# Performance work log

Hardware: AMD Instinct MI355X
Metric: run time of the kernel (lower is better)

## Reference

```python
import jax, jax.numpy as jnp
import numpy as np

B, S, EMB = 2, 2048, 4096
NHEADS, KVHEADS, HEAD_D = 32, 8, 128
SPLITS = (NHEADS * HEAD_D, KVHEADS * HEAD_D, KVHEADS * HEAD_D)  # 4096, 1024, 1024


def setup_inputs() -> dict:
    key = jax.random.key(0)
    k1, k2, k3 = jax.random.split(key, 3)
    q = jax.random.normal(k1, (B, S, EMB), dtype=jnp.float32)
    # nn.Linear weights, torch layout [out_features, in_features], std=0.02 init
    w_qkv = jax.random.normal(k2, (sum(SPLITS), EMB), dtype=jnp.float32) * 0.02
    w_dense = jax.random.normal(k3, (EMB, NHEADS * HEAD_D), dtype=jnp.float32) * 0.02
    return {"q": q, "w_qkv": w_qkv, "w_dense": w_dense}


def reference(q, w_qkv, w_dense):
    # Self-attention path of PagedMultiHeadAttention (no cache), causal mask.
    Bq, Sq, _ = q.shape
    qkv = q @ w_qkv.T                                  # [B, S, 6144]
    qs, ks, vs = jnp.split(qkv, np.cumsum(SPLITS)[:-1], axis=-1)
    G = NHEADS // KVHEADS                              # GQA expansion = 4
    # queries grouped per kv-head: [B, S, KVH, G, D]
    qh = qs.reshape(Bq, Sq, KVHEADS, G, HEAD_D)
    kh = ks.reshape(Bq, Sq, KVHEADS, HEAD_D)
    vh = vs.reshape(Bq, Sq, KVHEADS, HEAD_D)
    scale = 1.0 / jnp.sqrt(jnp.float32(HEAD_D))
    scores = jnp.einsum("bskgd,btkd->bkgst", qh, kh) * scale  # [B,KVH,G,S,S]
    causal = jnp.tril(jnp.ones((Sq, Sq), dtype=bool))
    scores = jnp.where(causal, scores, jnp.finfo(scores.dtype).min)
    probs = jax.nn.softmax(scores, axis=-1)
    attn = jnp.einsum("bkgst,btkd->bskgd", probs, vh)  # [B,S,KVH,G,D]
    attn = attn.reshape(Bq, Sq, NHEADS * HEAD_D)
    return attn @ w_dense.T                            # [B, S, EMB]
```

## Files before the change

kernel.cpp:

```cpp
#include <hip/hip_runtime.h>
#include <hip/hip_bf16.h>

typedef __bf16 bf16x8 __attribute__((ext_vector_type(8)));
typedef __bf16 bf16x4 __attribute__((ext_vector_type(4)));
typedef float  f32x4  __attribute__((ext_vector_type(4)));

typedef __attribute__((address_space(3))) void lds_vp;
typedef const __attribute__((address_space(1))) void gbl_vp;

__global__ void cast_f32_bf16(const float* __restrict__ src, __bf16* __restrict__ dst, int n8) {
    int i = blockIdx.x * 256 + threadIdx.x;
    if (i >= n8) return;
    const float4* s = (const float4*)src;
    float4 a = s[2 * i], b = s[2 * i + 1];
    bf16x8 o;
    o[0] = (__bf16)a.x; o[1] = (__bf16)a.y; o[2] = (__bf16)a.z; o[3] = (__bf16)a.w;
    o[4] = (__bf16)b.x; o[5] = (__bf16)b.y; o[6] = (__bf16)b.z; o[7] = (__bf16)b.w;
    ((bf16x8*)dst)[i] = o;
}


__device__ __forceinline__ void stage_half(const __bf16* __restrict__ g, int K, int kt,
                                           __bf16* lds_tile, int h, int w, int l) {
#pragma unroll
    for (int j = 0; j < 2; ++j) {
        const int rih = (j * 8 + w) * 8 + (l >> 3);
        const __bf16* src = g + (size_t)(h * 128 + rih) * K + kt * 64 + (((l & 7) ^ (l >> 3)) << 3);
        __bf16* dst = lds_tile + h * 8192 + (j * 8 + w) * 512;
        __builtin_amdgcn_global_load_lds((gbl_vp*)src, (lds_vp*)dst, 16, 0, 0);
    }
}

__device__ __forceinline__ bf16x8 lds_frag(const __bf16* base, int row, int kb) {
    return *(const bf16x8*)((const char*)base + row * 128 + (kb ^ ((row & 7) << 4)));
}

template <int OUT_BF16>
__global__ __launch_bounds__(512, 2)
void gemm256(const __bf16* __restrict__ A, const __bf16* __restrict__ Bm,
             void* __restrict__ Cout, int M, int N, int K) {
    __shared__ __bf16 As[2][256 * 64];
    __shared__ __bf16 Bs[2][256 * 64];
    const int tid = threadIdx.x;
    const int lane = tid & 63, wid = tid >> 6;
    const int g = lane >> 4, lq = lane & 15;
    const int wm = wid >> 2, wn = wid & 3;
    const size_t brow = (size_t)blockIdx.y * 256, bcol = (size_t)blockIdx.x * 256;
    const __bf16* Ag = A + brow * K;
    const __bf16* Bg = Bm + bcol * K;
    const int nkt = K >> 6, niter = nkt >> 1;

    f32x4 acc[8][4] = {};

    stage_half(Ag, K, 0, &As[0][0], 0, wid, lane);
    stage_half(Bg, K, 0, &Bs[0][0], 0, wid, lane);
    stage_half(Ag, K, 0, &As[0][0], 1, wid, lane);
    stage_half(Bg, K, 0, &Bs[0][0], 1, wid, lane);

    const int arow0 = wm * 128 + lq;
    const int brow0 = wn * 64 + lq;

    for (int it = 0; it < niter; ++it) {
        const int t0 = 2 * it;
#pragma unroll
        for (int hf = 0; hf < 2; ++hf) {
            const __bf16* SA = &As[hf][0];
            const __bf16* SB = &Bs[hf][0];
            __bf16* DA = &As[hf ^ 1][0];
            __bf16* DB = &Bs[hf ^ 1][0];
            const int tstage = t0 + 1 + hf;
            const bool dostage = (tstage < nkt);
            bf16x8 bfr[4][2];

            if (dostage) stage_half(Ag, K, tstage, DA, 0, wid, lane);
            __builtin_amdgcn_sched_barrier(0);
            if (dostage) asm volatile("s_waitcnt vmcnt(2)" ::: "memory");
            else         asm volatile("s_waitcnt vmcnt(0)" ::: "memory");
            __builtin_amdgcn_s_barrier();
            __builtin_amdgcn_sched_barrier(0);
#pragma unroll
            for (int n = 0; n < 4; ++n)
#pragma unroll
                for (int kk = 0; kk < 2; ++kk)
                    bfr[n][kk] = lds_frag(SB, brow0 + n * 16, kk * 64 + g * 16);
            {
                bf16x8 afr[2][2];
#pragma unroll
                for (int mm = 0; mm < 2; ++mm)
#pragma unroll
                    for (int kk = 0; kk < 2; ++kk)
                        afr[mm][kk] = lds_frag(SA, arow0 + mm * 16, kk * 64 + g * 16);
                __builtin_amdgcn_s_setprio(1);
#pragma unroll
                for (int kk = 0; kk < 2; ++kk)
#pragma unroll
                    for (int n = 0; n < 4; ++n)
#pragma unroll
                        for (int mm = 0; mm < 2; ++mm)
                            acc[mm][n] = __builtin_amdgcn_mfma_f32_16x16x32_bf16(afr[mm][kk], bfr[n][kk], acc[mm][n], 0, 0, 0);
                __builtin_amdgcn_s_setprio(0);
            }
            __builtin_amdgcn_sched_barrier(0);
            __builtin_amdgcn_s_barrier();
            __builtin_amdgcn_sched_barrier(0);

#pragma unroll
            for (int q = 1; q < 4; ++q) {
                bf16x8 afr[2][2];
#pragma unroll
                for (int mm = 0; mm < 2; ++mm)
#pragma unroll
                    for (int kk = 0; kk < 2; ++kk)
                        afr[mm][kk] = lds_frag(SA, arow0 + (q * 2 + mm) * 16, kk * 64 + g * 16);
                if (dostage) {
                    if (q == 1)      stage_half(Bg, K, tstage, DB, 0, wid, lane);
                    else if (q == 2) stage_half(Ag, K, tstage, DA, 1, wid, lane);
                    else             stage_half(Bg, K, tstage, DB, 1, wid, lane);
                }
                __builtin_amdgcn_sched_barrier(0);
                __builtin_amdgcn_s_barrier();
                __builtin_amdgcn_sched_barrier(0);
                __builtin_amdgcn_s_setprio(1);
#pragma unroll
                for (int kk = 0; kk < 2; ++kk)
#pragma unroll
                    for (int n = 0; n < 4; ++n)
#pragma unroll
                        for (int mm = 0; mm < 2; ++mm)
                            acc[q * 2 + mm][n] = __builtin_amdgcn_mfma_f32_16x16x32_bf16(afr[mm][kk], bfr[n][kk], acc[q * 2 + mm][n], 0, 0, 0);
                __builtin_amdgcn_s_setprio(0);
                __builtin_amdgcn_sched_barrier(0);
                __builtin_amdgcn_s_barrier();
                __builtin_amdgcn_sched_barrier(0);
            }
        }
    }

#pragma unroll
    for (int m = 0; m < 8; ++m) {
#pragma unroll
        for (int r = 0; r < 4; ++r) {
            size_t row = brow + wm * 128 + m * 16 + g * 4 + r;
#pragma unroll
            for (int n = 0; n < 4; ++n) {
                size_t col = bcol + wn * 64 + n * 16 + lq;
                float v = acc[m][n][r];
                if (OUT_BF16) ((__bf16*)Cout)[row * N + col] = (__bf16)v;
                else          ((float*)Cout)[row * N + col] = v;
            }
        }
    }
}

__global__ __launch_bounds__(256)
void transpose_v(const __bf16* __restrict__ qkv, __bf16* __restrict__ vt) {
    constexpr int S = 2048, QKVN = 6144;
    __shared__ __bf16 tile[64][72];
    const int tt = blockIdx.x;
    const int yz = blockIdx.y;
    const int dh = yz & 1, bkh = yz >> 1;
    const int b = bkh >> 3, kh = bkh & 7;
    const int tid = threadIdx.x;
#pragma unroll
    for (int i = 0; i < 2; ++i) {
        int flat = i * 2048 + tid * 8;
        int r = flat >> 6, c0 = flat & 63;
        const __bf16* src = qkv + ((size_t)b * S + tt * 64 + r) * QKVN + 5120 + kh * 128 + dh * 64 + c0;
        *(bf16x8*)&tile[r][c0] = *(const bf16x8*)src;
    }
    __syncthreads();
#pragma unroll
    for (int i = 0; i < 2; ++i) {
        int flat = i * 2048 + tid * 8;
        int d = flat >> 6, t0 = flat & 63;
        bf16x8 pk;
#pragma unroll
        for (int e = 0; e < 8; ++e) pk[e] = tile[t0 + e][d];
        __bf16* dst = vt + ((size_t)(b * 8 + kh) * 128 + dh * 64 + d) * S + tt * 64 + t0;
        *(bf16x8*)dst = pk;
    }
}

__global__ __launch_bounds__(256, 2)
void attn_kernel(const __bf16* __restrict__ qkv, const __bf16* __restrict__ vt,
                 __bf16* __restrict__ outb) {
    constexpr int S = 2048, D = 128, QKVN = 6144;
    const int p = blockIdx.x;
    const int kh = p & 7;
    const int j = p >> 3;
    const int qt = 15 - (j >> 3);
    const int b  = (j >> 2) & 1;
    const int g4 = j & 3;
    const int h  = kh * 4 + g4;
    const int tid = threadIdx.x, lane = tid & 63, w = tid >> 6;
    const int g = lane >> 4, lq = lane & 15;

    __shared__ __bf16 Ks[64 * 128];
    __shared__ __bf16 Vs[128 * 64];
    __shared__ char   PsRaw[4][2][16 * 152];

    const int wqmin = qt * 128 + w * 32;
    const int qg0 = wqmin + lq;
    const int qg1 = qg0 + 16;

    const __bf16* qrow = qkv + ((size_t)(b * S) + wqmin + lq) * QKVN + h * D;
    bf16x8 qf0[4], qf1[4];
#pragma unroll
    for (int ks = 0; ks < 4; ++ks) {
        qf0[ks] = *(const bf16x8*)(qrow + ks * 32 + g * 8);
        qf1[ks] = *(const bf16x8*)(qrow + (size_t)16 * QKVN + ks * 32 + g * 8);
    }

    const char* kbase = (const char*)qkv + ((size_t)(b * S) * QKVN + 4096 + kh * D) * 2;
    const char* vbase = (const char*)vt + ((size_t)(b * 8 + kh) * D * S) * 2;

    f32x4 acc0[8] = {}, acc1[8] = {};
    float m0 = -1e30f, l0 = 0.f, m1 = -1e30f, l1 = 0.f;
    const float scale2 = 0.12753102494f;

    const int krow0 = tid >> 4;
    const int kcolb = (tid & 15) * 16;
    const int vrow0 = tid >> 3;
    const int vcolb = (tid & 7) * 16;

    const int ktmax = 2 * qt + 1;
    int4 pk[4], pv[4];
#pragma unroll
    for (int is = 0; is < 4; ++is) {
        pk[is] = *(const int4*)(kbase + (size_t)(is * 16 + krow0) * QKVN * 2 + kcolb);
        pv[is] = *(const int4*)(vbase + (size_t)(is * 32 + vrow0) * S * 2 + vcolb);
    }

    char* ps0 = &PsRaw[w][0][0];
    char* ps1 = &PsRaw[w][1][0];

    for (int kt = 0; kt <= ktmax; ++kt) {
        __builtin_amdgcn_s_barrier();
#pragma unroll
        for (int is = 0; is < 4; ++is) {
            int row = is * 16 + krow0;
            *(int4*)((char*)Ks + row * 256 + (kcolb ^ ((row & 15) << 4))) = pk[is];
            int d = is * 32 + vrow0;
            *(int4*)((char*)Vs + d * 128 + (vcolb ^ ((d & 7) << 4))) = pv[is];
        }
        if (kt < ktmax) {
#pragma unroll
            for (int is = 0; is < 4; ++is) {
                pk[is] = *(const int4*)(kbase + (size_t)((kt + 1) * 64 + is * 16 + krow0) * QKVN * 2 + kcolb);
                pv[is] = *(const int4*)(vbase + ((size_t)(is * 32 + vrow0) * S + (kt + 1) * 64) * 2 + vcolb);
            }
        }
        __builtin_amdgcn_sched_barrier(0);
        asm volatile("s_waitcnt lgkmcnt(0)" ::: "memory");
        __builtin_amdgcn_sched_barrier(0);
        __builtin_amdgcn_s_barrier();
        __builtin_amdgcn_sched_barrier(0);

        if (kt * 64 <= wqmin + 31) {
            f32x4 sc0[4], sc1[4];
            __builtin_amdgcn_s_setprio(1);
#pragma unroll
            for (int tb = 0; tb < 4; ++tb) {
                f32x4 s0 = {0.f, 0.f, 0.f, 0.f}, s1 = {0.f, 0.f, 0.f, 0.f};
                const int trow = tb * 16 + lq;
                const int rsw = (trow & 15) << 4;
#pragma unroll
                for (int ks = 0; ks < 4; ++ks) {
                    bf16x8 kf = *(const bf16x8*)((const char*)Ks + trow * 256 + ((ks * 64 + g * 16) ^ rsw));
                    s0 = __builtin_amdgcn_mfma_f32_16x16x32_bf16(kf, qf0[ks], s0, 0, 0, 0);
                    s1 = __builtin_amdgcn_mfma_f32_16x16x32_bf16(kf, qf1[ks], s1, 0, 0, 0);
                }
                sc0[tb] = s0; sc1[tb] = s1;
            }
            __builtin_amdgcn_s_setprio(0);

#pragma unroll
            for (int f = 0; f < 2; ++f) {
                f32x4* sc = f ? sc1 : sc0;
                float& m_r = f ? m1 : m0;
                float& l_p = f ? l1 : l0;
                f32x4* acc = f ? acc1 : acc0;
                char* ps = f ? ps1 : ps0;
                const int qg = f ? qg1 : qg0;
                const bool domask = (kt * 64 + 63 > qg - lq);

                float pr[16];
                float rowmax = -1e30f;
#pragma unroll
                for (int tb = 0; tb < 4; ++tb)
#pragma unroll
                    for (int r = 0; r < 4; ++r) {
                        float sv = sc[tb][r] * scale2;
                        if (domask) {
                            int tg = kt * 64 + tb * 16 + g * 4 + r;
                            sv = (tg <= qg) ? sv : -1e30f;
                        }
                        pr[tb * 4 + r] = sv;
                        rowmax = fmaxf(rowmax, sv);
                    }
                rowmax = fmaxf(rowmax, __shfl_xor(rowmax, 16));
                rowmax = fmaxf(rowmax, __shfl_xor(rowmax, 32));
                if (!__all(rowmax - m_r <= 11.0f)) {
                    float m_new = fmaxf(m_r, rowmax);
                    float alpha = exp2f(m_r - m_new);
                    l_p *= alpha;
#pragma unroll
                    for (int r = 0; r < 4; ++r) {
                        float ar = __shfl(alpha, g * 4 + r);
#pragma unroll
                        for (int nb = 0; nb < 8; ++nb) acc[nb][r] *= ar;
                    }
                    m_r = m_new;
                }
                float lsum = 0.f;
#pragma unroll
                for (int i = 0; i < 16; ++i) {
                    float e = exp2f(pr[i] - m_r);
                    pr[i] = e;
                    lsum += e;
                }
                l_p += lsum;
#pragma unroll
                for (int tb = 0; tb < 4; ++tb) {
                    bf16x4 pkv;
#pragma unroll
                    for (int r = 0; r < 4; ++r) pkv[r] = (__bf16)pr[tb * 4 + r];
                    *(bf16x4*)(ps + lq * 152 + tb * 32 + g * 8) = pkv;
                }
            }

            __builtin_amdgcn_s_setprio(1);
#pragma unroll
            for (int ks = 0; ks < 2; ++ks) {
                bf16x8 pa0 = *(const bf16x8*)(ps0 + lq * 152 + ks * 64 + g * 16);
                bf16x8 pa1 = *(const bf16x8*)(ps1 + lq * 152 + ks * 64 + g * 16);
#pragma unroll
                for (int nb = 0; nb < 8; ++nb) {
                    int d = nb * 16 + lq;
                    bf16x8 vf = *(const bf16x8*)((const char*)Vs + d * 128 + ((ks * 64 + g * 16) ^ ((d & 7) << 4)));
                    acc0[nb] = __builtin_amdgcn_mfma_f32_16x16x32_bf16(pa0, vf, acc0[nb], 0, 0, 0);
                    acc1[nb] = __builtin_amdgcn_mfma_f32_16x16x32_bf16(pa1, vf, acc1[nb], 0, 0, 0);
                }
            }
            __builtin_amdgcn_s_setprio(0);
        }
        __builtin_amdgcn_sched_barrier(0);
    }

    l0 += __shfl_xor(l0, 16); l0 += __shfl_xor(l0, 32);
    l1 += __shfl_xor(l1, 16); l1 += __shfl_xor(l1, 32);
    float rl0 = 1.f / l0, rl1 = 1.f / l1;
#pragma unroll
    for (int r = 0; r < 4; ++r) {
        float rr0 = __shfl(rl0, g * 4 + r);
        float rr1 = __shfl(rl1, g * 4 + r);
        size_t row0 = (size_t)(b * S) + wqmin + g * 4 + r;
        __bf16* orow0 = outb + row0 * 4096 + h * D;
        __bf16* orow1 = orow0 + (size_t)16 * 4096;
#pragma unroll
        for (int nb = 0; nb < 8; ++nb) {
            orow0[nb * 16 + lq] = (__bf16)(acc0[nb][r] * rr0);
            orow1[nb * 16 + lq] = (__bf16)(acc1[nb][r] * rr1);
        }
    }
}

extern "C" void kernel_launch(void* const* d_in, const int* in_sizes, int n_in,
                              void* d_out, int out_size, void* d_ws, size_t ws_size,
                              hipStream_t stream) {
    (void)in_sizes; (void)n_in; (void)out_size; (void)ws_size;
    const float* q       = (const float*)d_in[0];
    const float* w_qkv   = (const float*)d_in[1];
    const float* w_dense = (const float*)d_in[2];
    float* out = (float*)d_out;
    char* ws = (char*)d_ws;

    __bf16* qbf      = (__bf16*)(ws);
    __bf16* wqkvbf   = (__bf16*)(ws + 33554432ULL);
    __bf16* wdensebf = (__bf16*)(ws + 83886080ULL);
    __bf16* qkvbf    = (__bf16*)(ws + 117440512ULL);
    __bf16* vtbf     = (__bf16*)(ws + 167772160ULL);
    __bf16* attnbf   = (__bf16*)(ws + 176160768ULL);

    cast_f32_bf16<<<8192, 256, 0, stream>>>(q, qbf, 2097152);
    cast_f32_bf16<<<12288, 256, 0, stream>>>(w_qkv, wqkvbf, 3145728);
    cast_f32_bf16<<<8192, 256, 0, stream>>>(w_dense, wdensebf, 2097152);

    gemm256<1><<<dim3(24, 16), 512, 0, stream>>>(qbf, wqkvbf, (void*)qkvbf, 4096, 6144, 4096);
    transpose_v<<<dim3(32, 32), 256, 0, stream>>>(qkvbf, vtbf);
    attn_kernel<<<1024, 256, 0, stream>>>(qkvbf, vtbf, attnbf);
    gemm256<0><<<dim3(16, 16), 512, 0, stream>>>(attnbf, wdensebf, (void*)out, 4096, 4096, 4096);
}
```

Baseline: 677.0 us.

## Replace QKV projection GEMM with 128x128-tile kernel and swizzled block order

The QKV projection now uses a new 128x128-tile, 256-thread GEMM instead of the 256x256, 512-thread kernel. It stages tiles through registers into XOR-swizzled LDS, and it remaps block IDs across 8 groups to improve L2 locality. This gives 1536 blocks instead of 384, so the 256 CUs get more even wave coverage. The cost is lower data reuse per tile, and the synchronous global-to-LDS staging has no double buffering, so memory latency is exposed on every K step.

```diff
diff --git a/kernel.cpp b/kernel.cpp
--- a/kernel.cpp
+++ b/kernel.cpp
@@ -19,6 +19,74 @@
     ((bf16x8*)dst)[i] = o;
 }
 
+template <int OUT_BF16>
+__global__ __launch_bounds__(256)
+void gemm_bt(const __bf16* __restrict__ A, const __bf16* __restrict__ Bm,
+             void* __restrict__ Cout, int M, int N, int K, int ntx) {
+    __shared__ __bf16 As[128 * 64];
+    __shared__ __bf16 Bs[128 * 64];
+    const int p = blockIdx.x;
+    const int cpx = gridDim.x >> 3;
+    const int swz = (p & 7) * cpx + (p >> 3);
+    const int bx = swz % ntx, by = swz / ntx;
+    const int tid = threadIdx.x;
+    const int lane = tid & 63, wid = tid >> 6;
+    const int g = lane >> 4, lq = lane & 15;
+    const int wr = wid >> 1, wc = wid & 1;
+    const size_t brow = (size_t)by * 128, bcol = (size_t)bx * 128;
+    f32x4 acc[4][4] = {};
+    const int nkt = K >> 6;
+
+    for (int kt = 0; kt < nkt; ++kt) {
+        __syncthreads();
+#pragma unroll
+        for (int is = 0; is < 4; ++is) {
+            int flat = is * 4096 + tid * 16;
+            int row  = flat >> 7;
+            int colb = flat & 127;
+            int sw   = colb ^ ((row & 7) << 4);
+            int4 va = *(const int4*)((const char*)A + ((brow + row) * (size_t)K + (size_t)kt * 64) * 2 + colb);
+            *(int4*)((char*)As + row * 128 + sw) = va;
+            int4 vb = *(const int4*)((const char*)Bm + ((bcol + row) * (size_t)K + (size_t)kt * 64) * 2 + colb);
+            *(int4*)((char*)Bs + row * 128 + sw) = vb;
+        }
+        __syncthreads();
+#pragma unroll
+        for (int ks = 0; ks < 2; ++ks) {
+            bf16x8 af[4], bfr[4];
+            const int kb = ks * 64 + g * 16;
+#pragma unroll
+            for (int i = 0; i < 4; ++i) {
+                int row = wr * 64 + i * 16 + lq;
+                af[i] = *(const bf16x8*)((const char*)As + row * 128 + (kb ^ ((row & 7) << 4)));
+            }
+#pragma unroll
+            for (int j = 0; j < 4; ++j) {
+                int row = wc * 64 + j * 16 + lq;
+                bfr[j] = *(const bf16x8*)((const char*)Bs + row * 128 + (kb ^ ((row & 7) << 4)));
+            }
+#pragma unroll
+            for (int i = 0; i < 4; ++i)
+#pragma unroll
+                for (int j = 0; j < 4; ++j)
+                    acc[i][j] = __builtin_amdgcn_mfma_f32_16x16x32_bf16(af[i], bfr[j], acc[i][j], 0, 0, 0);
+        }
+    }
+#pragma unroll
+    for (int i = 0; i < 4; ++i) {
+#pragma unroll
+        for (int r = 0; r < 4; ++r) {
+            size_t row = brow + wr * 64 + i * 16 + g * 4 + r;
+#pragma unroll
+            for (int j = 0; j < 4; ++j) {
+                size_t col = bcol + wc * 64 + j * 16 + lq;
+                float v = acc[i][j][r];
+                if (OUT_BF16) ((__bf16*)Cout)[row * N + col] = (__bf16)v;
+                else          ((float*)Cout)[row * N + col] = v;
+            }
+        }
+    }
+}
 
 __device__ __forceinline__ void stage_half(const __bf16* __restrict__ g, int K, int kt,
                                            __bf16* lds_tile, int h, int w, int l) {
@@ -386,7 +454,7 @@
     cast_f32_bf16<<<12288, 256, 0, stream>>>(w_qkv, wqkvbf, 3145728);
     cast_f32_bf16<<<8192, 256, 0, stream>>>(w_dense, wdensebf, 2097152);
 
-    gemm256<1><<<dim3(24, 16), 512, 0, stream>>>(qbf, wqkvbf, (void*)qkvbf, 4096, 6144, 4096);
+    gemm_bt<1><<<1536, 256, 0, stream>>>(qbf, wqkvbf, (void*)qkvbf, 4096, 6144, 4096, 48);
     transpose_v<<<dim3(32, 32), 256, 0, stream>>>(qkvbf, vtbf);
     attn_kernel<<<1024, 256, 0, stream>>>(qkvbf, vtbf, attnbf);
     gemm256<0><<<dim3(16, 16), 512, 0, stream>>>(attnbf, wdensebf, (void*)out, 4096, 4096, 4096);
```

Result: no change. 678.9 us (+0.3%).
